# Kernel tuning notes

Hardware: AMD Instinct MI355X
Metric: run time of the kernel (lower is better)

Reference implementation:

```python
import jax, jax.numpy as jnp
import numpy as np

B, C, H, W = 4, 64, 64, 64


def setup_inputs() -> dict:
    key = jax.random.key(0)
    ks = jax.random.split(key, 9)
    s = 1.0 / np.sqrt(C)
    return {
        "x1": jax.random.normal(ks[0], (B, C, H, W), dtype=jnp.float32),
        "x2": jax.random.normal(ks[1], (B, C, H, W), dtype=jnp.float32),
        "wq": jax.random.normal(ks[2], (C, C), dtype=jnp.float32) * s,
        "bq": jax.random.normal(ks[3], (C,), dtype=jnp.float32) * 0.01,
        "wk": jax.random.normal(ks[4], (C, C), dtype=jnp.float32) * s,
        "bk": jax.random.normal(ks[5], (C,), dtype=jnp.float32) * 0.01,
        "wv": jax.random.normal(ks[6], (C, C), dtype=jnp.float32) * s,
        "bv": jax.random.normal(ks[7], (C,), dtype=jnp.float32) * 0.01,
        "gamma": jax.random.normal(ks[8], (1,), dtype=jnp.float32) * 0.1,
    }


def _conv1x1(x, w, b):
    # 1x1 conv == per-pixel GEMM: [B,C,H,W] x [Cout,Cin] -> [B,Cout,H,W]
    return jnp.einsum('bchw,oc->bohw', x, w) + b[None, :, None, None]


def reference(x1, x2, wq, bq, wk, bk, wv, bv, gamma):
    b, c, h, w = x1.shape
    n = h * w
    q = _conv1x1(x1, wq, bq).reshape(b, c, n)   # [B,C,N]
    k = _conv1x1(x2, wk, bk).reshape(b, c, n)   # [B,C,N]
    v = _conv1x1(x2, wv, bv).reshape(b, c, n)   # [B,C,N]
    # attention[b,i,j] = sum_c q[b,c,i] * k[b,c,j]  -> [B,N,N]
    attn = jnp.einsum('bci,bcj->bij', q, k)
    attn = jax.nn.softmax(attn, axis=-1)
    # out[b,c,i] = sum_j v[b,c,j] * attn[b,i,j]
    out = jnp.einsum('bcj,bij->bci', v, attn).reshape(b, c, h, w)
    return gamma[0] * out + x1
```

## Files before the change

### kernel.cpp

```cpp
#include <hip/hip_runtime.h>
#include <cstdint>
#include <cstddef>


typedef __bf16 bf16x2 __attribute__((ext_vector_type(2)));
typedef __bf16 bf16x4 __attribute__((ext_vector_type(4)));
typedef __bf16 bf16x8 __attribute__((ext_vector_type(8)));
typedef float  f32x4  __attribute__((ext_vector_type(4)));
typedef float  f32x16 __attribute__((ext_vector_type(16)));

constexpr int C = 64;
constexpr int N = 4096;
constexpr float LOG2E = 1.44269504088896340736f;

static __device__ __forceinline__ f32x4 mfma16(bf16x8 a, bf16x8 b, f32x4 c) {
    return __builtin_amdgcn_mfma_f32_16x16x32_bf16(a, b, c, 0, 0, 0);
}
static __device__ __forceinline__ f32x16 mfma32(bf16x8 a, bf16x8 b, f32x16 c) {
    return __builtin_amdgcn_mfma_f32_32x32x16_bf16(a, b, c, 0, 0, 0);
}
static __device__ __forceinline__ float fast_exp2(float x) {
#if __has_builtin(__builtin_amdgcn_exp2f)
    return __builtin_amdgcn_exp2f(x);
#else
    return exp2f(x);
#endif
}
static __device__ __forceinline__ uint32_t pack2(float a, float b) {
    union { uint32_t u; bf16x2 h; } w;
    w.h = bf16x2{(__bf16)a, (__bf16)b};
    return w.u;
}

__global__ __launch_bounds__(256) void qkv_kernel(
    const float* __restrict__ x1, const float* __restrict__ x2,
    const float* __restrict__ wq, const float* __restrict__ bq,
    const float* __restrict__ wk, const float* __restrict__ bk,
    const float* __restrict__ wv, const float* __restrict__ bv,
    __bf16* __restrict__ qo, __bf16* __restrict__ ko, __bf16* __restrict__ vo)
{
    __shared__ __bf16 wl[2][64][72];
    __shared__ __bf16 tout[64][72];

    const int bid  = blockIdx.x;
    const int kv   = bid >> 8;
    const int pg   = bid & 255;
    const int b     = pg >> 6;
    const int nbase = (pg & 63) * 64;
    const int tid   = threadIdx.x;

    const float* xsel = kv ? x2 : x1;

    {
        const float* w0 = kv ? wk : wq;
#pragma unroll
        for (int i = 0; i < 4; ++i) {
            int idx = i * 256 + tid;
            int row = idx >> 4, c4 = (idx & 15) * 4;
            float4 a = *(const float4*)(w0 + row * 64 + c4);
            bf16x4 h = {(__bf16)a.x, (__bf16)a.y, (__bf16)a.z, (__bf16)a.w};
            *(bf16x4*)&wl[0][row][c4] = h;
        }
        if (kv) {
#pragma unroll
            for (int i = 0; i < 4; ++i) {
                int idx = i * 256 + tid;
                int row = idx >> 4, c4 = (idx & 15) * 4;
                float4 a = *(const float4*)(wv + row * 64 + c4);
                bf16x4 h = {(__bf16)a.x, (__bf16)a.y, (__bf16)a.z, (__bf16)a.w};
                *(bf16x4*)&wl[1][row][c4] = h;
            }
        }
    }
    __syncthreads();

    const int wave = tid >> 6, lane = tid & 63;
    const int l = lane & 15, qd = lane >> 4;
    const int p = nbase + wave * 16 + l;

    const float* xb = xsel + (size_t)b * C * N + p;
    bf16x8 ax[2];
#pragma unroll
    for (int ks = 0; ks < 2; ++ks)
#pragma unroll
        for (int j = 0; j < 8; ++j)
            ax[ks][j] = (__bf16)xb[(size_t)(ks * 32 + qd * 8 + j) * N];

    {
        const float* bsel = kv ? bk : bq;
        __bf16*      osel = kv ? ko : qo;
        const float scale = kv ? 1.0f : LOG2E;
#pragma unroll
        for (int ot = 0; ot < 4; ++ot) {
            const float bb = bsel[ot * 16 + l];
            f32x4 acc = {bb, bb, bb, bb};
#pragma unroll
            for (int ks = 0; ks < 2; ++ks) {
                bf16x8 bw = *(const bf16x8*)&wl[0][ot * 16 + l][ks * 32 + qd * 8];
                acc = mfma16(ax[ks], bw, acc);
            }
#pragma unroll
            for (int r = 0; r < 4; ++r) {
                int px = wave * 16 + qd * 4 + r;
                tout[px][ot * 16 + l] = (__bf16)(acc[r] * scale);
            }
        }
        __syncthreads();

        const int tile = tid >> 7, t7 = tid & 127;
        const int kc = t7 >> 5, h2 = (t7 >> 4) & 1, ilp = (t7 & 15) * 2;
        const size_t tb = ((size_t)b * 128 + (nbase >> 5) + tile) * 2048;
        const size_t off = tb + kc * 512 + h2 * 256 + ilp * 8;
        bf16x8 ra = *(const bf16x8*)&tout[tile * 32 + ilp][kc * 16 + h2 * 8];
        bf16x8 rb = *(const bf16x8*)&tout[tile * 32 + ilp + 1][kc * 16 + h2 * 8];
        *(bf16x8*)&osel[off]     = ra;
        *(bf16x8*)&osel[off + 8] = rb;
    }

    if (!kv) return;

    __syncthreads();
#pragma unroll
    for (int ct = 0; ct < 4; ++ct) {
        f32x4 acc;
#pragma unroll
        for (int r = 0; r < 4; ++r) acc[r] = bv[ct * 16 + qd * 4 + r];
#pragma unroll
        for (int ks = 0; ks < 2; ++ks) {
            bf16x8 aw = *(const bf16x8*)&wl[1][ct * 16 + l][ks * 32 + qd * 8];
            acc = mfma16(aw, ax[ks], acc);
        }
        bf16x4 pk = {(__bf16)acc[0], (__bf16)acc[1], (__bf16)acc[2], (__bf16)acc[3]};
        *(bf16x4*)&tout[wave * 16 + l][ct * 16 + qd * 4] = pk;
    }
    __syncthreads();

    {
        const int tile = tid >> 7, t7 = tid & 127;
        const int G = t7 >> 6, vh = (t7 >> 5) & 1, il = t7 & 31;
        const int pxb = tile * 32 + G * 16 + vh * 8;
        bf16x8 oA, oB;
#pragma unroll
        for (int e = 0; e < 8; ++e) {
            oA[e] = tout[pxb + e][il];
            oB[e] = tout[pxb + e][32 + il];
        }
        const size_t tb = ((size_t)b * 128 + (nbase >> 5) + tile) * 2048;
        const size_t off = tb + G * 1024 + vh * 512 + (size_t)il * 16;
        *(bf16x8*)&vo[off]     = oA;
        *(bf16x8*)&vo[off + 8] = oB;
    }
}

__global__ __launch_bounds__(512, 2) void attn_kernel(
    const __bf16* __restrict__ qg, const __bf16* __restrict__ kg,
    const __bf16* __restrict__ vg, const float* __restrict__ x1,
    const float* __restrict__ gamma, float* __restrict__ out)
{
    __shared__ float lds_acc[3][64][64];
    __shared__ float lds_l[8][64];

    const int bid = blockIdx.x;
    const int xcd = bid & 7;
    const int b   = xcd >> 1;
    const int rt  = ((bid >> 3) << 1) | (xcd & 1);
    const int ibase = rt * 64;

    const int tid  = threadIdx.x;
    const int wave = tid >> 6, lane = tid & 63;
    const int il = lane & 31, hi = lane >> 5;

    const __bf16* qt = qg + ((size_t)b * 128 + rt * 2) * 2048;
    const __bf16* kt = kg + (size_t)b * 128 * 2048 + (size_t)(wave * 16) * 2048;
    const __bf16* vt = vg + (size_t)b * 128 * 2048 + (size_t)(wave * 16) * 2048;

    bf16x8 bqf[2][4];
#pragma unroll
    for (int qs = 0; qs < 2; ++qs)
#pragma unroll
        for (int kc = 0; kc < 4; ++kc)
            bqf[qs][kc] = *(const bf16x8*)(qt + qs * 2048 + kc * 512 + lane * 8);

    f32x16 zf;
#pragma unroll
    for (int r = 0; r < 16; ++r) zf[r] = 0.f;

    f32x16 accO[4];
#pragma unroll
    for (int a = 0; a < 4; ++a)
#pragma unroll
        for (int r = 0; r < 16; ++r) accO[a][r] = 0.f;
    float lsum[2] = {0.f, 0.f};

    bf16x8 akf[2][4];
    bf16x8 avf[2][2][2];

#pragma unroll
    for (int kc = 0; kc < 4; ++kc)
        akf[0][kc] = *(const bf16x8*)(kt + kc * 512 + lane * 8);
#pragma unroll
    for (int ct = 0; ct < 2; ++ct)
#pragma unroll
        for (int G = 0; G < 2; ++G)
            avf[0][ct][G] = *(const bf16x8*)(vt + G * 1024 + hi * 512 + il * 16 + ct * 8);

#pragma unroll 2
    for (int t = 0; t < 16; ++t) {
        const int cur = t & 1;
        if (t < 15) {
            const size_t nb = (size_t)(t + 1) * 2048;
#pragma unroll
            for (int kc = 0; kc < 4; ++kc)
                akf[cur ^ 1][kc] = *(const bf16x8*)(kt + nb + kc * 512 + lane * 8);
#pragma unroll
            for (int ct = 0; ct < 2; ++ct)
#pragma unroll
                for (int G = 0; G < 2; ++G)
                    avf[cur ^ 1][ct][G] = *(const bf16x8*)(vt + nb + G * 1024 + hi * 512 + il * 16 + ct * 8);
        }

#pragma unroll
        for (int qs = 0; qs < 2; ++qs) {
            __builtin_amdgcn_s_setprio(1);
            f32x16 st = mfma32(akf[cur][0], bqf[qs][0], zf);
#pragma unroll
            for (int kc = 1; kc < 4; ++kc) st = mfma32(akf[cur][kc], bqf[qs][kc], st);
            __builtin_amdgcn_s_setprio(0);

            float e0, e1;
            float lp0 = 0.f, lp1 = 0.f;
            uint32_t a0, a1, b0, b1, c0, c1, d0, d1;
            e0 = fast_exp2(st[0]);  e1 = fast_exp2(st[1]);
            lp0 += e0; lp1 += e1; a0 = pack2(e0, e1);
            e0 = fast_exp2(st[2]);  e1 = fast_exp2(st[3]);
            lp0 += e0; lp1 += e1; a1 = pack2(e0, e1);
            e0 = fast_exp2(st[4]);  e1 = fast_exp2(st[5]);
            lp0 += e0; lp1 += e1; b0 = pack2(e0, e1);
            e0 = fast_exp2(st[6]);  e1 = fast_exp2(st[7]);
            lp0 += e0; lp1 += e1; b1 = pack2(e0, e1);
            e0 = fast_exp2(st[8]);  e1 = fast_exp2(st[9]);
            lp0 += e0; lp1 += e1; c0 = pack2(e0, e1);
            e0 = fast_exp2(st[10]); e1 = fast_exp2(st[11]);
            lp0 += e0; lp1 += e1; c1 = pack2(e0, e1);
            e0 = fast_exp2(st[12]); e1 = fast_exp2(st[13]);
            lp0 += e0; lp1 += e1; d0 = pack2(e0, e1);
            e0 = fast_exp2(st[14]); e1 = fast_exp2(st[15]);
            lp0 += e0; lp1 += e1; d1 = pack2(e0, e1);
            lsum[qs] += lp0 + lp1;

            asm("v_permlane32_swap_b32 %0, %1" : "+v"(a0), "+v"(b0));
            asm("v_permlane32_swap_b32 %0, %1" : "+v"(a1), "+v"(b1));
            asm("v_permlane32_swap_b32 %0, %1" : "+v"(c0), "+v"(d0));
            asm("v_permlane32_swap_b32 %0, %1" : "+v"(c1), "+v"(d1));
            union F { uint32_t u[4]; bf16x8 v; } f0, f1;
            f0.u[0] = a0; f0.u[1] = a1; f0.u[2] = b0; f0.u[3] = b1;
            f1.u[0] = c0; f1.u[1] = c1; f1.u[2] = d0; f1.u[3] = d1;

            __builtin_amdgcn_s_setprio(1);
#pragma unroll
            for (int ct = 0; ct < 2; ++ct) {
                accO[qs * 2 + ct] = mfma32(avf[cur][ct][0], f0.v, accO[qs * 2 + ct]);
                accO[qs * 2 + ct] = mfma32(avf[cur][ct][1], f1.v, accO[qs * 2 + ct]);
            }
            __builtin_amdgcn_s_setprio(0);
        }
    }

#pragma unroll
    for (int qs = 0; qs < 2; ++qs) lsum[qs] += __shfl_xor(lsum[qs], 32);
    if (hi == 0) {
        lds_l[wave][il]      = lsum[0];
        lds_l[wave][32 + il] = lsum[1];
    }

#define ACC_STORE(SLOT)                                                        \
    do {                                                                       \
        _Pragma("unroll")                                                      \
        for (int qs = 0; qs < 2; ++qs)                                         \
            _Pragma("unroll")                                                  \
            for (int ct = 0; ct < 2; ++ct)                                     \
                _Pragma("unroll")                                              \
                for (int r = 0; r < 16; ++r)                                   \
                    lds_acc[SLOT][ct * 32 + (r & 3) + 8 * (r >> 2) + 4 * hi][qs * 32 + il] = accO[qs * 2 + ct][r]; \
    } while (0)
#define ACC_LOAD(SLOT)                                                         \
    do {                                                                       \
        _Pragma("unroll")                                                      \
        for (int qs = 0; qs < 2; ++qs)                                         \
            _Pragma("unroll")                                                  \
            for (int ct = 0; ct < 2; ++ct)                                     \
                _Pragma("unroll")                                              \
                for (int r = 0; r < 16; ++r)                                   \
                    accO[qs * 2 + ct][r] += lds_acc[SLOT][ct * 32 + (r & 3) + 8 * (r >> 2) + 4 * hi][qs * 32 + il]; \
    } while (0)

    if (wave >= 5) ACC_STORE(wave - 5);
    __syncthreads();
    if (wave >= 1 && wave <= 3) ACC_LOAD(wave - 1);
    __syncthreads();
    if (wave >= 2 && wave <= 4) ACC_STORE(wave - 2);
    __syncthreads();
    if (wave <= 1) ACC_LOAD(wave);
    if (wave == 0) ACC_LOAD(2);
    __syncthreads();
    if (wave == 1) ACC_STORE(0);
    __syncthreads();
    if (wave == 0) { ACC_LOAD(0); ACC_STORE(0); }
    __syncthreads();
#undef ACC_STORE
#undef ACC_LOAD

    const float g = gamma[0];
    {
        const int c  = tid >> 3;
        const int i8 = (tid & 7) * 8;
        float lv[8];
#pragma unroll
        for (int e = 0; e < 8; ++e) {
            float s = 0.f;
#pragma unroll
            for (int w = 0; w < 8; ++w) s += lds_l[w][i8 + e];
            lv[e] = s;
        }
        const size_t idx = ((size_t)b * C + c) * N + ibase + i8;
        f32x4 o0 = *(const f32x4*)&lds_acc[0][c][i8];
        f32x4 o1 = *(const f32x4*)&lds_acc[0][c][i8 + 4];
        f32x4 x0 = *(const f32x4*)(x1 + idx);
        f32x4 x4 = *(const f32x4*)(x1 + idx + 4);
        f32x4 r0, r1;
#pragma unroll
        for (int e = 0; e < 4; ++e) {
            r0[e] = g * o0[e] / lv[e] + x0[e];
            r1[e] = g * o1[e] / lv[4 + e] + x4[e];
        }
        *(f32x4*)(out + idx) = r0;
        *(f32x4*)(out + idx + 4) = r1;
    }
}

extern "C" void kernel_launch(void* const* d_in, const int* in_sizes, int n_in,
                              void* d_out, int out_size, void* d_ws, size_t ws_size,
                              hipStream_t stream) {
    const float* x1    = (const float*)d_in[0];
    const float* x2    = (const float*)d_in[1];
    const float* wq    = (const float*)d_in[2];
    const float* bqv   = (const float*)d_in[3];
    const float* wk    = (const float*)d_in[4];
    const float* bkv   = (const float*)d_in[5];
    const float* wv    = (const float*)d_in[6];
    const float* bvv   = (const float*)d_in[7];
    const float* gamma = (const float*)d_in[8];
    float* out = (float*)d_out;

    __bf16* qws = (__bf16*)d_ws;
    __bf16* kws = qws + (size_t)4 * 128 * 2048;
    __bf16* vws = kws + (size_t)4 * 128 * 2048;

    qkv_kernel<<<512, 256, 0, stream>>>(x1, x2, wq, bqv, wk, bkv, wv, bvv, qws, kws, vws);
    attn_kernel<<<256, 512, 0, stream>>>(qws, kws, vws, x1, gamma, out);
}
```

Measured before the change: 100.1 us.

## Fuse Q projection into attention kernel and drop setprio hints

Computes the Q 1x1-conv projection inside the attention kernel instead of the separate QKV kernel. Each block loads wq into LDS, projects its own 64 query pixels from x1, and reads the Q fragments from LDS, so Q is never written to or read back from global memory. The first kernel now launches only the K/V half of the grid. It also removes the s_setprio hints around the MFMA sections. The cost is extra prologue work and syncs in the attention kernel, which reuses the accumulator LDS space as scratch.

```diff
diff --git a/kernel.cpp b/kernel.cpp
--- a/kernel.cpp
+++ b/kernel.cpp
@@ -32,45 +32,30 @@
     return w.u;
 }
 
-__global__ __launch_bounds__(256) void qkv_kernel(
-    const float* __restrict__ x1, const float* __restrict__ x2,
-    const float* __restrict__ wq, const float* __restrict__ bq,
+__global__ __launch_bounds__(256) void kv_kernel(
+    const float* __restrict__ x2,
     const float* __restrict__ wk, const float* __restrict__ bk,
     const float* __restrict__ wv, const float* __restrict__ bv,
-    __bf16* __restrict__ qo, __bf16* __restrict__ ko, __bf16* __restrict__ vo)
+    __bf16* __restrict__ ko, __bf16* __restrict__ vo)
 {
     __shared__ __bf16 wl[2][64][72];
     __shared__ __bf16 tout[64][72];
 
-    const int bid  = blockIdx.x;
-    const int kv   = bid >> 8;
-    const int pg   = bid & 255;
+    const int pg   = blockIdx.x;
     const int b     = pg >> 6;
     const int nbase = (pg & 63) * 64;
     const int tid   = threadIdx.x;
 
-    const float* xsel = kv ? x2 : x1;
-
-    {
-        const float* w0 = kv ? wk : wq;
-#pragma unroll
-        for (int i = 0; i < 4; ++i) {
-            int idx = i * 256 + tid;
-            int row = idx >> 4, c4 = (idx & 15) * 4;
-            float4 a = *(const float4*)(w0 + row * 64 + c4);
-            bf16x4 h = {(__bf16)a.x, (__bf16)a.y, (__bf16)a.z, (__bf16)a.w};
-            *(bf16x4*)&wl[0][row][c4] = h;
-        }
-        if (kv) {
-#pragma unroll
-            for (int i = 0; i < 4; ++i) {
-                int idx = i * 256 + tid;
-                int row = idx >> 4, c4 = (idx & 15) * 4;
-                float4 a = *(const float4*)(wv + row * 64 + c4);
-                bf16x4 h = {(__bf16)a.x, (__bf16)a.y, (__bf16)a.z, (__bf16)a.w};
-                *(bf16x4*)&wl[1][row][c4] = h;
-            }
-        }
+#pragma unroll
+    for (int i = 0; i < 4; ++i) {
+        int idx = i * 256 + tid;
+        int row = idx >> 4, c4 = (idx & 15) * 4;
+        float4 a = *(const float4*)(wk + row * 64 + c4);
+        bf16x4 h = {(__bf16)a.x, (__bf16)a.y, (__bf16)a.z, (__bf16)a.w};
+        *(bf16x4*)&wl[0][row][c4] = h;
+        float4 av = *(const float4*)(wv + row * 64 + c4);
+        bf16x4 hv = {(__bf16)av.x, (__bf16)av.y, (__bf16)av.z, (__bf16)av.w};
+        *(bf16x4*)&wl[1][row][c4] = hv;
     }
     __syncthreads();
 
@@ -78,7 +63,7 @@
     const int l = lane & 15, qd = lane >> 4;
     const int p = nbase + wave * 16 + l;
 
-    const float* xb = xsel + (size_t)b * C * N + p;
+    const float* xb = x2 + (size_t)b * C * N + p;
     bf16x8 ax[2];
 #pragma unroll
     for (int ks = 0; ks < 2; ++ks)
@@ -87,12 +72,9 @@
             ax[ks][j] = (__bf16)xb[(size_t)(ks * 32 + qd * 8 + j) * N];
 
     {
-        const float* bsel = kv ? bk : bq;
-        __bf16*      osel = kv ? ko : qo;
-        const float scale = kv ? 1.0f : LOG2E;
 #pragma unroll
         for (int ot = 0; ot < 4; ++ot) {
-            const float bb = bsel[ot * 16 + l];
+            const float bb = bk[ot * 16 + l];
             f32x4 acc = {bb, bb, bb, bb};
 #pragma unroll
             for (int ks = 0; ks < 2; ++ks) {
@@ -102,7 +84,7 @@
 #pragma unroll
             for (int r = 0; r < 4; ++r) {
                 int px = wave * 16 + qd * 4 + r;
-                tout[px][ot * 16 + l] = (__bf16)(acc[r] * scale);
+                tout[px][ot * 16 + l] = (__bf16)acc[r];
             }
         }
         __syncthreads();
@@ -113,11 +95,9 @@
         const size_t off = tb + kc * 512 + h2 * 256 + ilp * 8;
         bf16x8 ra = *(const bf16x8*)&tout[tile * 32 + ilp][kc * 16 + h2 * 8];
         bf16x8 rb = *(const bf16x8*)&tout[tile * 32 + ilp + 1][kc * 16 + h2 * 8];
-        *(bf16x8*)&osel[off]     = ra;
-        *(bf16x8*)&osel[off + 8] = rb;
-    }
-
-    if (!kv) return;
+        *(bf16x8*)&ko[off]     = ra;
+        *(bf16x8*)&ko[off + 8] = rb;
+    }
 
     __syncthreads();
 #pragma unroll
@@ -153,8 +133,9 @@
 }
 
 __global__ __launch_bounds__(512, 2) void attn_kernel(
-    const __bf16* __restrict__ qg, const __bf16* __restrict__ kg,
-    const __bf16* __restrict__ vg, const float* __restrict__ x1,
+    const __bf16* __restrict__ kg, const __bf16* __restrict__ vg,
+    const float* __restrict__ x1,
+    const float* __restrict__ wq, const float* __restrict__ bq,
     const float* __restrict__ gamma, float* __restrict__ out)
 {
     __shared__ float lds_acc[3][64][64];
@@ -170,16 +151,59 @@
     const int wave = tid >> 6, lane = tid & 63;
     const int il = lane & 31, hi = lane >> 5;
 
-    const __bf16* qt = qg + ((size_t)b * 128 + rt * 2) * 2048;
+    __bf16* wl_q   = (__bf16*)&lds_acc[0][0][0];
+    __bf16* tout_q = wl_q + 64 * 72;
+
+    {
+#pragma unroll
+        for (int i = 0; i < 2; ++i) {
+            int idx = i * 512 + tid;
+            int row = idx >> 4, c4 = (idx & 15) * 4;
+            float4 a = *(const float4*)(wq + row * 64 + c4);
+            bf16x4 h = {(__bf16)a.x, (__bf16)a.y, (__bf16)a.z, (__bf16)a.w};
+            *(bf16x4*)&wl_q[row * 72 + c4] = h;
+        }
+    }
+    __syncthreads();
+
+    if (wave < 4) {
+        const int l = lane & 15, qd = lane >> 4;
+        const int p = ibase + wave * 16 + l;
+        const float* xb = x1 + (size_t)b * C * N + p;
+        bf16x8 ax[2];
+#pragma unroll
+        for (int ks = 0; ks < 2; ++ks)
+#pragma unroll
+            for (int j = 0; j < 8; ++j)
+                ax[ks][j] = (__bf16)xb[(size_t)(ks * 32 + qd * 8 + j) * N];
+#pragma unroll
+        for (int ot = 0; ot < 4; ++ot) {
+            const float bb = bq[ot * 16 + l];
+            f32x4 acc = {bb, bb, bb, bb};
+#pragma unroll
+            for (int ks = 0; ks < 2; ++ks) {
+                bf16x8 bw = *(const bf16x8*)&wl_q[(ot * 16 + l) * 72 + ks * 32 + qd * 8];
+                acc = mfma16(ax[ks], bw, acc);
+            }
+#pragma unroll
+            for (int r = 0; r < 4; ++r) {
+                int px = wave * 16 + qd * 4 + r;
+                tout_q[px * 72 + ot * 16 + l] = (__bf16)(acc[r] * LOG2E);
+            }
+        }
+    }
+    __syncthreads();
+
+    bf16x8 bqf[2][4];
+#pragma unroll
+    for (int qs = 0; qs < 2; ++qs)
+#pragma unroll
+        for (int kc = 0; kc < 4; ++kc)
+            bqf[qs][kc] = *(const bf16x8*)&tout_q[(qs * 32 + il) * 72 + kc * 16 + hi * 8];
+    __syncthreads();
+
     const __bf16* kt = kg + (size_t)b * 128 * 2048 + (size_t)(wave * 16) * 2048;
     const __bf16* vt = vg + (size_t)b * 128 * 2048 + (size_t)(wave * 16) * 2048;
-
-    bf16x8 bqf[2][4];
-#pragma unroll
-    for (int qs = 0; qs < 2; ++qs)
-#pragma unroll
-        for (int kc = 0; kc < 4; ++kc)
-            bqf[qs][kc] = *(const bf16x8*)(qt + qs * 2048 + kc * 512 + lane * 8);
 
     f32x16 zf;
 #pragma unroll
@@ -221,11 +245,9 @@
 
 #pragma unroll
         for (int qs = 0; qs < 2; ++qs) {
-            __builtin_amdgcn_s_setprio(1);
             f32x16 st = mfma32(akf[cur][0], bqf[qs][0], zf);
 #pragma unroll
             for (int kc = 1; kc < 4; ++kc) st = mfma32(akf[cur][kc], bqf[qs][kc], st);
-            __builtin_amdgcn_s_setprio(0);
 
             float e0, e1;
             float lp0 = 0.f, lp1 = 0.f;
@@ -256,13 +278,11 @@
             f0.u[0] = a0; f0.u[1] = a1; f0.u[2] = b0; f0.u[3] = b1;
             f1.u[0] = c0; f1.u[1] = c1; f1.u[2] = d0; f1.u[3] = d1;
 
-            __builtin_amdgcn_s_setprio(1);
 #pragma unroll
             for (int ct = 0; ct < 2; ++ct) {
                 accO[qs * 2 + ct] = mfma32(avf[cur][ct][0], f0.v, accO[qs * 2 + ct]);
                 accO[qs * 2 + ct] = mfma32(avf[cur][ct][1], f1.v, accO[qs * 2 + ct]);
             }
-            __builtin_amdgcn_s_setprio(0);
         }
     }
 
@@ -352,10 +372,9 @@
     const float* gamma = (const float*)d_in[8];
     float* out = (float*)d_out;
 
-    __bf16* qws = (__bf16*)d_ws;
-    __bf16* kws = qws + (size_t)4 * 128 * 2048;
+    __bf16* kws = (__bf16*)d_ws;
     __bf16* vws = kws + (size_t)4 * 128 * 2048;
 
-    qkv_kernel<<<512, 256, 0, stream>>>(x1, x2, wq, bqv, wk, bkv, wv, bvv, qws, kws, vws);
-    attn_kernel<<<256, 512, 0, stream>>>(qws, kws, vws, x1, gamma, out);
-}
+    kv_kernel<<<256, 256, 0, stream>>>(x2, wk, bkv, wv, bvv, kws, vws);
+    attn_kernel<<<256, 512, 0, stream>>>(kws, vws, x1, wq, bqv, gamma, out);
+}
```

New measurement: 101.2 us. No clear change (+1.1%).
